# Optimization experiments

Hardware: AMD Instinct MI355X
Metric: run time of the kernel (lower is better)

## Reference

```python
import jax, jax.numpy as jnp
import numpy as np

B = 16        # graphs per protein batch
NPG = 2000    # nodes per graph
N = B * NPG   # total nodes
E = 640000    # total edges
H, C = 3, 128 # heads, hidden_dim
FIN = 1038
K = 400       # ceil(0.2 * NPG) SAGPool keep count
NEG = 0.1     # LeakyReLU slope in model
EPS = 1e-5


def setup_inputs() -> dict:
    key = jax.random.key(0)
    ks = jax.random.split(key, 24)
    d = {}
    d['p1_x'] = jax.random.normal(ks[0], (N, FIN), jnp.float32)
    d['p2_x'] = jax.random.normal(ks[1], (N, FIN), jnp.float32)
    d['p1_edge_index'] = jax.random.randint(ks[2], (2, E), 0, N, jnp.int32)
    d['p2_edge_index'] = jax.random.randint(ks[3], (2, E), 0, N, jnp.int32)
    d['p1_edge_attr'] = jax.random.uniform(ks[4], (E, 2), jnp.float32)
    d['p2_edge_attr'] = jax.random.uniform(ks[5], (E, 2), jnp.float32)
    s_in = 1.0 / np.sqrt(FIN)
    s_h = 1.0 / np.sqrt(C)
    # GATv2Conv params (lin_l has bias, lin_r no bias, lin_edge, att, out bias)
    d['Wl'] = jax.random.normal(ks[6], (FIN, H * C), jnp.float32) * s_in
    d['bl'] = jnp.zeros((H * C,), jnp.float32)
    d['Wr'] = jax.random.normal(ks[7], (FIN, H * C), jnp.float32) * s_in
    d['We'] = jax.random.normal(ks[8], (2, H * C), jnp.float32) * 0.5
    d['att'] = jax.random.normal(ks[9], (H, C), jnp.float32) * s_h
    d['conv_bias'] = jnp.zeros((C,), jnp.float32)
    # BatchNorm1d
    d['gamma'] = jnp.ones((C,), jnp.float32)
    d['beta'] = jnp.zeros((C,), jnp.float32)
    # SAGPooling scorer: GraphConv(C -> 1)
    d['gc_Wrel'] = jax.random.normal(ks[10], (C, 1), jnp.float32) * s_h
    d['gc_Wroot'] = jax.random.normal(ks[11], (C, 1), jnp.float32) * s_h
    d['gc_b'] = jnp.zeros((1,), jnp.float32)
    # MLP head
    d['W1'] = jax.random.normal(ks[12], (2 * C, C), jnp.float32) / np.sqrt(2 * C)
    d['b1'] = jnp.zeros((C,), jnp.float32)
    d['W2'] = jax.random.normal(ks[13], (C, C // 2), jnp.float32) * s_h
    d['b2'] = jnp.zeros((C // 2,), jnp.float32)
    d['Wo'] = jax.random.normal(ks[14], (C // 2, 1), jnp.float32) / np.sqrt(C // 2)
    d['bo'] = jnp.zeros((1,), jnp.float32)
    return d


def gatv2(x, ei, ea, Wl, bl, Wr, We, att, conv_bias):
    # GATv2Conv, heads=3, concat=False, edge_dim=2, add_self_loops (fill='mean')
    loop = jnp.arange(N, dtype=ei.dtype)
    src = jnp.concatenate([ei[0], loop])
    dst = jnp.concatenate([ei[1], loop])
    ea_full = jnp.concatenate([ea, jnp.broadcast_to(ea.mean(0), (N, ea.shape[1]))], 0)
    xl = (x @ Wl + bl).reshape(N, H, C)
    xr = (x @ Wr).reshape(N, H, C)
    ef = (ea_full @ We).reshape(-1, H, C)
    m = xl[src] + xr[dst] + ef                      # [E+N, H, C]
    e = jnp.einsum('ehc,hc->eh', jax.nn.leaky_relu(m, 0.2), att)
    emax = jax.ops.segment_max(e, dst, num_segments=N)
    ex = jnp.exp(e - emax[dst])
    denom = jax.ops.segment_sum(ex, dst, num_segments=N)
    alpha = ex / denom[dst]                          # softmax per dst node, per head
    out = jax.ops.segment_sum(alpha[:, :, None] * xl[src], dst, num_segments=N)
    return out.mean(1) + conv_bias                   # concat=False -> head mean


def branch(x, ei, ea, Wl, bl, Wr, We, att, conv_bias, gamma, beta,
           gc_Wrel, gc_Wroot, gc_b):
    h = gatv2(x, ei, ea, Wl, bl, Wr, We, att, conv_bias)
    h = jax.nn.leaky_relu(h, NEG)
    mu = h.mean(0)
    var = ((h - mu) ** 2).mean(0)
    h = (h - mu) / jnp.sqrt(var + EPS) * gamma + beta  # BatchNorm1d (batch stats)
    # SAGPooling scorer: GraphConv out_i = W_root x_i + W_rel sum_{j->i} x_j + b
    agg = jax.ops.segment_sum(h[ei[0]], ei[1], num_segments=N)
    score = jnp.tanh((h @ gc_Wroot + agg @ gc_Wrel + gc_b)[:, 0])  # [N]
    s = score.reshape(B, NPG)
    topv, topi = jax.lax.top_k(s, K)                 # per-graph top-k
    hb = h.reshape(B, NPG, C)
    hsel = jnp.take_along_axis(hb, topi[:, :, None], axis=1)  # [B, K, C]
    hsel = hsel * topv[:, :, None]                   # x[perm] * tanh(score)[perm]
    return hsel.mean(1)                              # global mean pool -> [B, C]


def reference(p1_x, p2_x, p1_edge_attr, p2_edge_attr, Wl, bl, Wr, We, att,
              conv_bias, gamma, beta, gc_Wrel, gc_Wroot, gc_b, W1, b1, W2, b2,
              Wo, bo, p1_edge_index, p2_edge_index):
    x1 = branch(p1_x, p1_edge_index, p1_edge_attr, Wl, bl, Wr, We, att,
                conv_bias, gamma, beta, gc_Wrel, gc_Wroot, gc_b)
    x2 = branch(p2_x, p2_edge_index, p2_edge_attr, Wl, bl, Wr, We, att,
                conv_bias, gamma, beta, gc_Wrel, gc_Wroot, gc_b)
    xc = jnp.concatenate([x1, x2], 1)                # [B, 2C]
    xc = jax.nn.leaky_relu(xc @ W1 + b1, NEG)
    xc = jax.nn.leaky_relu(xc @ W2 + b2, NEG)
    return jax.nn.sigmoid(xc @ Wo + bo)              # [B, 1]
```

## Files before the change

kernel.cpp:

```cpp
#include <hip/hip_runtime.h>
#include <hip/hip_bf16.h>
#include <math.h>

#define NN 32000
#define EE 640000
#define CC 128
#define HC 384
#define FIN 1038
#define KP 1056
#define KT 33
#define BB 16
#define NPG 2000
#define KK 400

#define XLR_STR 12288000u
#define HBN_STR 4096000u
#define OFF_STR 32064u

#define XL_OFF     0u
#define XR_OFF     24576000u
#define HBN_OFF    49152000u
#define SSRC_OFF   57344000u
#define SEA_OFF    58624000u
#define CNT_OFF    61184000u
#define BNSUM_OFF  61248000u
#define BNSQ_OFF   61248256u
#define MEANEA_OFF 61248512u
#define ZERO_BYTES ((61248516u - 61184000u) * 4u)
#define OFFS_OFF   61248576u
#define CUR_OFF    61312704u
#define R_OFF      61376704u
#define REL_OFF    61440704u
#define SCORE_OFF  61504704u
#define XB_OFF     61568704u
#define WTH_OFF    61572800u

typedef __attribute__((ext_vector_type(8))) _Float16 f16x8;
typedef __attribute__((ext_vector_type(2))) _Float16 f16x2;
typedef __attribute__((ext_vector_type(4))) float f32x4;
typedef __attribute__((ext_vector_type(8))) unsigned short us8;

typedef const __attribute__((address_space(1))) unsigned int* gp1_t;
typedef __attribute__((address_space(3))) unsigned int* lp3_t;
__device__ __forceinline__ void gl_lds16(const void* g, void* l) {
    __builtin_amdgcn_global_load_lds((gp1_t)g, (lp3_t)l, 16, 0, 0);
}

__global__ __launch_bounds__(256) void k_prep(const int* __restrict__ ei0, const int* __restrict__ ei1,
                                              const float* __restrict__ ea0, const float* __restrict__ ea1,
                                              int* __restrict__ cnt, float* __restrict__ meanea) {
    int b = blockIdx.x;
    int br = (b >= 2500);
    int tid = threadIdx.x;
    int e = (b - br * 2500) * 256 + tid;
    const int* ei = br ? ei1 : ei0;
    const float* ea = br ? ea1 : ea0;
    cnt += br * NN; meanea += br * 2;
    float s0 = 0.f, s1 = 0.f;
    if (e < EE) {
        atomicAdd(&cnt[ei[EE + e]], 1);
        float2 t = ((const float2*)ea)[e];
        s0 = t.x; s1 = t.y;
    }
    __shared__ float r0[256], r1[256];
    r0[tid] = s0; r1[tid] = s1; __syncthreads();
    for (int st = 128; st; st >>= 1) {
        if (tid < st) { r0[tid] += r0[tid + st]; r1[tid] += r1[tid + st]; }
        __syncthreads();
    }
    if (tid == 0) { atomicAdd(&meanea[0], r0[0]); atomicAdd(&meanea[1], r1[0]); }
}

__global__ __launch_bounds__(1024) void k_scan(const int* __restrict__ cnt, int* __restrict__ offs, int* __restrict__ cur) {
    int br = blockIdx.x;
    cnt += br * NN; offs += br * OFF_STR; cur += br * NN;
    __shared__ int sb[1024];
    int tid = threadIdx.x;
    int base = tid * 32;
    int s = 0;
    for (int i = 0; i < 32; i++) { int idx = base + i; s += (idx < NN) ? cnt[idx] : 0; }
    sb[tid] = s; __syncthreads();
    for (int off = 1; off < 1024; off <<= 1) {
        int v = (tid >= off) ? sb[tid - off] : 0;
        __syncthreads();
        sb[tid] += v;
        __syncthreads();
    }
    int run = sb[tid] - s;
    for (int i = 0; i < 32; i++) {
        int idx = base + i;
        if (idx < NN) { int c = cnt[idx]; offs[idx] = run; cur[idx] = run; run += c; }
    }
    if (tid == 1023) offs[NN] = run;
}

__global__ __launch_bounds__(256) void k_scatter(const int* __restrict__ ei0, const int* __restrict__ ei1,
                                                 const float* __restrict__ ea0, const float* __restrict__ ea1,
                                                 int* __restrict__ cur, int* __restrict__ ssrc, float2* __restrict__ sea) {
    int b = blockIdx.x;
    int br = (b >= 2500);
    int e = (b - br * 2500) * 256 + threadIdx.x;
    const int* ei = br ? ei1 : ei0;
    const float* ea = br ? ea1 : ea0;
    cur += br * NN; ssrc += br * EE; sea += br * EE;
    if (e < EE) {
        int d = ei[EE + e];
        int p = atomicAdd(&cur[d], 1);
        ssrc[p] = ei[e];
        sea[p] = ((const float2*)ea)[e];
    }
}

__global__ __launch_bounds__(256) void k_cvtW(const float* __restrict__ Wl_, const float* __restrict__ Wr_,
                                              unsigned short* __restrict__ Bh) {
    int idx = blockIdx.x * 256 + threadIdx.x;
    if (idx >= 768 * (KP / 8)) return;
    int n = idx / (KP / 8);
    int seg = idx - n * (KP / 8);
    int c0 = seg * 8;
    const float* W = (n < HC) ? Wl_ : Wr_;
    int nc = (n < HC) ? n : n - HC;
    us8 h8;
#pragma unroll
    for (int j = 0; j < 8; ++j) {
        int k = c0 + j;
        float v = (k < FIN) ? W[(size_t)k * HC + nc] : 0.f;
        _Float16 h = (_Float16)v;
        h8[j] = __builtin_bit_cast(unsigned short, h);
    }
    *(us8*)&Bh[(size_t)n * KP + c0] = h8;
}

__global__ __launch_bounds__(256) void k_gemm2f(const float* __restrict__ x0, const float* __restrict__ x1,
                                                const unsigned short* __restrict__ Bh,
                                                const float* __restrict__ bias, float* __restrict__ ws) {
    __shared__ _Float16 sA[128 * 32], sB[128 * 32];
    const int bid = blockIdx.x;
    const int br = (bid >= 1504);
    const int b2 = br ? (bid - 1504) : bid;
    const float* x = br ? x1 : x0;
    _Float16* xlh = (_Float16*)(ws + XL_OFF) + (size_t)br * XLR_STR;
    float* xr = ws + XR_OFF + br * XLR_STR;

    const int xcd = b2 & 7, slot = b2 >> 3;
    const int t = xcd * 188 + slot;
    if (t >= 1500) return;
    const int mt = t / 6, nt = t - mt * 6;
    const int bm = mt * 128, bn = nt * 128;

    const int tid = threadIdx.x;
    const int wave = tid >> 6, lane = tid & 63;
    const int wm = (wave >> 1) * 64, wn = (wave & 1) * 64;
    const int quad = lane >> 4, l15 = lane & 15;

    const int srow = wave * 16 + (lane >> 2);
    const int scol = (lane & 3) * 8;
    const size_t gB0 = (size_t)(bn + srow) * KP + scol;
    const size_t gB1 = (size_t)(bn + 64 + srow) * KP + scol;
    const int lB0 = (wave * 16) * 32 + lane * 8;
    const int lB1 = (64 + wave * 16) * 32 + lane * 8;

    const int arow0 = wave * 32 + (lane >> 2);
    const int acol = (lane & 3) * 8;

    f32x4 acc[4][4];
#pragma unroll
    for (int i = 0; i < 4; ++i)
#pragma unroll
        for (int j = 0; j < 4; ++j) {
            f32x4 z = {0.f, 0.f, 0.f, 0.f};
            acc[i][j] = z;
        }

    const int aoff0 = (wm + l15) * 32 + quad * 8;
    const int boff0 = (wn + l15) * 32 + quad * 8;

    for (int kt = 0; kt < KT; ++kt) {
        const int kc = kt * 32;
        gl_lds16(Bh + gB0 + kc, &sB[lB0]);
        gl_lds16(Bh + gB1 + kc, &sB[lB1]);
        int gcol = kc + acol;
        if (gcol >= FIN) gcol = 0;
#pragma unroll
        for (int rep = 0; rep < 2; ++rep) {
            const int lrow = arow0 + rep * 16;
            const float* gp = x + (size_t)(bm + lrow) * FIN + gcol;
            float2 v01 = ((const float2*)gp)[0];
            float2 v23 = ((const float2*)gp)[1];
            float2 v45 = ((const float2*)gp)[2];
            float2 v67 = ((const float2*)gp)[3];
            f16x8 a;
            a[0] = (_Float16)v01.x; a[1] = (_Float16)v01.y;
            a[2] = (_Float16)v23.x; a[3] = (_Float16)v23.y;
            a[4] = (_Float16)v45.x; a[5] = (_Float16)v45.y;
            a[6] = (_Float16)v67.x; a[7] = (_Float16)v67.y;
            const int lidx = lrow * 32 + acol;
            *(f16x8*)&sA[lidx] = a;
        }
        __syncthreads();
        f16x8 b[4];
#pragma unroll
        for (int j = 0; j < 4; ++j) b[j] = *(const f16x8*)&sB[boff0 + j * 512];
#pragma unroll
        for (int i = 0; i < 4; ++i) {
            f16x8 a = *(const f16x8*)&sA[aoff0 + i * 512];
#pragma unroll
            for (int j = 0; j < 4; ++j)
                acc[i][j] = __builtin_amdgcn_mfma_f32_16x16x32_f16(a, b[j], acc[i][j], 0, 0, 0);
        }
        __syncthreads();
    }

    const bool isL = (nt < 3);
    if (isL) {
#pragma unroll
        for (int j = 0; j < 4; ++j) {
            const int ncol = wn + j * 16 + l15;
            const float bj = bias[bn + ncol];
#pragma unroll
            for (int i = 0; i < 4; ++i) {
#pragma unroll
                for (int r = 0; r < 4; ++r) {
                    int m = bm + wm + i * 16 + quad * 4 + r;
                    xlh[(size_t)m * HC + bn + ncol] = (_Float16)(acc[i][j][r] + bj);
                }
            }
        }
    } else {
        const int nbase = bn - HC;
#pragma unroll
        for (int j = 0; j < 4; ++j) {
            const int ncol = wn + j * 16 + l15;
#pragma unroll
            for (int i = 0; i < 4; ++i) {
#pragma unroll
                for (int r = 0; r < 4; ++r) {
                    int m = bm + wm + i * 16 + quad * 4 + r;
                    xr[(size_t)m * HC + nbase + ncol] = acc[i][j][r];
                }
            }
        }
    }
}

__global__ __launch_bounds__(256) void k_gat(const unsigned short* __restrict__ xlhb, const float* __restrict__ xrb,
                                             const int* __restrict__ offsb, const int* __restrict__ ssrcb,
                                             const float2* __restrict__ seab, const float* __restrict__ meaneab,
                                             const float* __restrict__ We, const float* __restrict__ att,
                                             const float* __restrict__ conv_bias, float* __restrict__ houtb) {
    int gwave = (blockIdx.x * 256 + threadIdx.x) >> 6;
    int lane = threadIdx.x & 63;
    int half = lane >> 5, l32 = lane & 31;
    int br = (gwave >= NN);
    int node = gwave - br * NN;
    const _Float16* xlh = (const _Float16*)xlhb + (size_t)br * XLR_STR;
    const float* xr = xrb + br * XLR_STR;
    const int* offs = offsb + br * OFF_STR;
    const int* ssrc = ssrcb + br * EE;
    const float2* sea = seab + br * EE;
    const float* meanea = meaneab + br * 2;
    float* hout = houtb + br * HBN_STR;

    f16x2 we0p[6], we1p[6], attp[6], xrp[6];
    const float2* xrw = (const float2*)(xr + (size_t)node * HC);
#pragma unroll
    for (int jj = 0; jj < 6; ++jj) {
        int q = l32 + 32 * jj;
        float2 w0 = ((const float2*)We)[q];
        float2 w1 = ((const float2*)(We + HC))[q];
        float2 av = ((const float2*)att)[q];
        float2 xv = xrw[q];
        we0p[jj][0] = (_Float16)w0.x; we0p[jj][1] = (_Float16)w0.y;
        we1p[jj][0] = (_Float16)w1.x; we1p[jj][1] = (_Float16)w1.y;
        attp[jj][0] = (_Float16)av.x; attp[jj][1] = (_Float16)av.y;
        xrp[jj][0]  = (_Float16)xv.x; xrp[jj][1]  = (_Float16)xv.y;
    }
    float me0 = meanea[0] * (1.0f / EE), me1 = meanea[1] * (1.0f / EE);

    int p0 = offs[node], p1 = offs[node + 1];
    int cntE = p1 - p0;
    int iters = (cntE + 2) >> 1;

    float den0 = 0.f, den1 = 0.f, den2 = 0.f;
    float accv[12];
#pragma unroll
    for (int k = 0; k < 12; ++k) accv[k] = 0.f;

    const f16x2 zero2 = {(_Float16)0.f, (_Float16)0.f};
    const f16x2 c02 = {(_Float16)0.2f, (_Float16)0.2f};

    for (int i = 0; i < iters; ++i) {
        int t = 2 * i + half;
        bool self = (t == 0);
        bool valid = (t <= cntE);
        int p = p0 + t - 1;
        if (p < p0) p = p0;
        if (p > EE - 1) p = EE - 1;
        int sv = ssrc[p];
        float2 ev = sea[p];
        int s = self ? node : sv;
        float ea0 = self ? me0 : ev.x;
        float ea1 = self ? me1 : ev.y;
        f16x2 e0p, e1p;
        e0p[0] = (_Float16)ea0; e0p[1] = e0p[0];
        e1p[0] = (_Float16)ea1; e1p[1] = e1p[0];

        const f16x2* xrow = (const f16x2*)(xlh + (size_t)s * HC);
        f16x2 xv[6];
#pragma unroll
        for (int jj = 0; jj < 6; ++jj) xv[jj] = xrow[l32 + 32 * jj];

        float pr0 = 0.f, pr1 = 0.f, pr2 = 0.f;
#pragma unroll
        for (int jj = 0; jj < 6; ++jj) {
            f16x2 u = xrp[jj] + e0p * we0p[jj];
            u = u + e1p * we1p[jj];
            f16x2 m = xv[jj] + u;
            f16x2 mx = __builtin_elementwise_max(m, zero2);
            f16x2 mn = __builtin_elementwise_min(m, zero2);
            f16x2 lk = mx + mn * c02;
#if __has_builtin(__builtin_amdgcn_fdot2)
            if (jj < 2)      pr0 = __builtin_amdgcn_fdot2(lk, attp[jj], pr0, false);
            else if (jj < 4) pr1 = __builtin_amdgcn_fdot2(lk, attp[jj], pr1, false);
            else             pr2 = __builtin_amdgcn_fdot2(lk, attp[jj], pr2, false);
#else
            float c = (float)lk[0] * (float)attp[jj][0] + (float)lk[1] * (float)attp[jj][1];
            if (jj < 2) pr0 += c; else if (jj < 4) pr1 += c; else pr2 += c;
#endif
        }
#pragma unroll
        for (int msk = 16; msk; msk >>= 1) {
            pr0 += __shfl_xor(pr0, msk);
            pr1 += __shfl_xor(pr1, msk);
            pr2 += __shfl_xor(pr2, msk);
        }
        float w0 = valid ? __expf(pr0) : 0.f;
        float w1 = valid ? __expf(pr1) : 0.f;
        float w2 = valid ? __expf(pr2) : 0.f;
        den0 += w0; den1 += w1; den2 += w2;
#pragma unroll
        for (int jj = 0; jj < 6; ++jj) {
            float wh = (jj < 2) ? w0 : ((jj < 4) ? w1 : w2);
            accv[2 * jj]     += wh * (float)xv[jj][0];
            accv[2 * jj + 1] += wh * (float)xv[jj][1];
        }
    }

#pragma unroll
    for (int k = 0; k < 12; ++k) accv[k] += __shfl_xor(accv[k], 32);
    den0 += __shfl_xor(den0, 32);
    den1 += __shfl_xor(den1, 32);
    den2 += __shfl_xor(den2, 32);

    if (half == 0) {
        float i0 = 1.f / den0, i1 = 1.f / den1, i2 = 1.f / den2;
#pragma unroll
        for (int jja = 0; jja < 2; ++jja) {
#pragma unroll
            for (int b = 0; b < 2; ++b) {
                int c = (((jja * 32 + l32) << 1) | b);
                float o = (accv[2 * jja + b] * i0 + accv[2 * (jja + 2) + b] * i1 +
                           accv[2 * (jja + 4) + b] * i2) * (1.f / 3.f) + conv_bias[c];
                o = (o > 0.f) ? o : 0.1f * o;
                hout[(size_t)node * CC + c] = o;
            }
        }
    }
}

__global__ __launch_bounds__(256) void k_bnstats(const float* __restrict__ hb, float* __restrict__ bnsumb, float* __restrict__ bnsqb) {
    int b = blockIdx.x;
    int br = b >> 9, lb = b & 511;
    const float* h = hb + br * HBN_STR;
    float* bnsum = bnsumb + br * CC;
    float* bnsq = bnsqb + br * CC;
    int c = threadIdx.x & 127;
    int row0 = lb * 2 + (threadIdx.x >> 7);
    float s = 0.f, ss = 0.f;
    for (int n = row0; n < NN; n += 1024) {
        float v = h[(size_t)n * CC + c];
        s += v; ss += v * v;
    }
    atomicAdd(&bnsum[c], s);
    atomicAdd(&bnsq[c], ss);
}

__global__ __launch_bounds__(256) void k_bnapply(float* __restrict__ hb, const float* __restrict__ bnsumb,
                                                 const float* __restrict__ bnsqb,
                                                 const float* __restrict__ gamma, const float* __restrict__ beta,
                                                 const float* __restrict__ wroot,
                                                 const float* __restrict__ wrel, float* __restrict__ r_b, float* __restrict__ rel_b) {
    int gwave = (blockIdx.x * 256 + threadIdx.x) >> 6;
    int lane = threadIdx.x & 63;
    int br = (gwave >= NN);
    int wave = gwave - br * NN;
    float* h = hb + br * HBN_STR;
    const float* bnsum = bnsumb + br * CC;
    const float* bnsq = bnsqb + br * CC;
    float* r_ = r_b + br * NN;
    float* rel_ = rel_b + br * NN;

    float mu0 = bnsum[lane] * (1.f / NN);
    float var0 = bnsq[lane] * (1.f / NN) - mu0 * mu0;
    float sc0 = gamma[lane] * rsqrtf(var0 + 1e-5f);
    float sh0 = beta[lane] - mu0 * sc0;
    float mu1 = bnsum[64 + lane] * (1.f / NN);
    float var1 = bnsq[64 + lane] * (1.f / NN) - mu1 * mu1;
    float sc1 = gamma[64 + lane] * rsqrtf(var1 + 1e-5f);
    float sh1 = beta[64 + lane] - mu1 * sc1;

    size_t base = (size_t)wave * CC;
    float v0 = h[base + lane], v1 = h[base + 64 + lane];
    v0 = v0 * sc0 + sh0;
    v1 = v1 * sc1 + sh1;
    h[base + lane] = v0;
    h[base + 64 + lane] = v1;
    float pr = v0 * wroot[lane] + v1 * wroot[64 + lane];
    float pl = v0 * wrel[lane] + v1 * wrel[64 + lane];
#pragma unroll
    for (int m = 32; m; m >>= 1) {
        pr += __shfl_xor(pr, m);
        pl += __shfl_xor(pl, m);
    }
    if (lane == 0) { r_[wave] = pr; rel_[wave] = pl; }
}

__global__ __launch_bounds__(256) void k_score(const float* __restrict__ r_b, const float* __restrict__ rel_b,
                                               const int* __restrict__ offsb, const int* __restrict__ ssrcb,
                                               const float* __restrict__ gcb, float* __restrict__ scoreb) {
    int gwave = (blockIdx.x * 256 + threadIdx.x) >> 6;
    int lane = threadIdx.x & 63;
    int br = (gwave >= NN);
    int wave = gwave - br * NN;
    const float* r_ = r_b + br * NN;
    const float* rel_ = rel_b + br * NN;
    const int* offs = offsb + br * OFF_STR;
    const int* ssrc = ssrcb + br * EE;
    float* score = scoreb + br * NN;
    int p0 = offs[wave], p1 = offs[wave + 1];
    float s = 0.f;
    for (int p = p0 + lane; p < p1; p += 64) s += rel_[ssrc[p]];
#pragma unroll
    for (int m = 32; m; m >>= 1) s += __shfl_xor(s, m);
    if (lane == 0) score[wave] = tanhf(r_[wave] + s + gcb[0]);
}

__global__ __launch_bounds__(1024) void k_topk(const float* __restrict__ scoreb, const float* __restrict__ hb,
                                               float* __restrict__ xbout) {
    __shared__ float sv[2048];
    __shared__ int si[2048];
    __shared__ float red[8][128];
    int b = blockIdx.x, tid = threadIdx.x;
    int br = b >> 4, g = b & 15;
    const float* score = scoreb + br * NN;
    const float* h = hb + br * HBN_STR;
    for (int i = tid; i < 2048; i += 1024) {
        sv[i] = (i < NPG) ? score[g * NPG + i] : -2.0f;
        si[i] = i;
    }
    __syncthreads();
    for (int k = 2; k <= 2048; k <<= 1) {
        for (int j = k >> 1; j > 0; j >>= 1) {
            for (int t = tid; t < 2048; t += 1024) {
                int ixj = t ^ j;
                if (ixj > t) {
                    bool up = ((t & k) == 0);
                    float a = sv[t], bv = sv[ixj];
                    bool sw = up ? (a < bv) : (a > bv);
                    if (sw) {
                        sv[t] = bv; sv[ixj] = a;
                        int tmp = si[t]; si[t] = si[ixj]; si[ixj] = tmp;
                    }
                }
            }
            __syncthreads();
        }
    }
    int grp = tid >> 7, c = tid & 127;
    float a = 0.f;
    for (int kk = grp; kk < KK; kk += 8) {
        int node = g * NPG + si[kk];
        a += sv[kk] * h[(size_t)node * CC + c];
    }
    red[grp][c] = a;
    __syncthreads();
    if (tid < 128) {
        float v = (red[0][tid] + red[1][tid] + red[2][tid] + red[3][tid] +
                   red[4][tid] + red[5][tid] + red[6][tid] + red[7][tid]) * (1.f / KK);
        xbout[(br * BB + g) * CC + tid] = v;
    }
}

__global__ __launch_bounds__(128) void k_mlp(const float* __restrict__ xb, const float* __restrict__ W1,
                                             const float* __restrict__ b1, const float* __restrict__ W2,
                                             const float* __restrict__ b2, const float* __restrict__ Wo,
                                             const float* __restrict__ bo, float* __restrict__ out) {
    int g = blockIdx.x, tid = threadIdx.x;
    __shared__ float xc[256], l1[128], l2[64];
    xc[tid] = xb[g * CC + tid];
    xc[128 + tid] = xb[BB * CC + g * CC + tid];
    __syncthreads();
    float s = b1[tid];
    for (int i = 0; i < 256; i++) s += xc[i] * W1[i * 128 + tid];
    l1[tid] = (s > 0.f) ? s : 0.1f * s;
    __syncthreads();
    if (tid < 64) {
        float s2 = b2[tid];
        for (int i = 0; i < 128; i++) s2 += l1[i] * W2[i * 64 + tid];
        l2[tid] = (s2 > 0.f) ? s2 : 0.1f * s2;
    }
    __syncthreads();
    if (tid < 64) {
        float p = l2[tid] * Wo[tid];
#pragma unroll
        for (int m = 32; m; m >>= 1) p += __shfl_xor(p, m);
        if (tid == 0) out[g] = 1.f / (1.f + __expf(-(p + bo[0])));
    }
}

extern "C" void kernel_launch(void* const* d_in, const int* in_sizes, int n_in,
                              void* d_out, int out_size, void* d_ws, size_t ws_size,
                              hipStream_t stream) {
    (void)in_sizes; (void)n_in; (void)out_size; (void)ws_size;
    const float* x0   = (const float*)d_in[0];
    const float* x1   = (const float*)d_in[1];
    const int*   ei0  = (const int*)d_in[2];
    const int*   ei1  = (const int*)d_in[3];
    const float* ea0  = (const float*)d_in[4];
    const float* ea1  = (const float*)d_in[5];
    const float* Wl   = (const float*)d_in[6];
    const float* bl   = (const float*)d_in[7];
    const float* Wr   = (const float*)d_in[8];
    const float* We   = (const float*)d_in[9];
    const float* att  = (const float*)d_in[10];
    const float* cb   = (const float*)d_in[11];
    const float* gam  = (const float*)d_in[12];
    const float* bet  = (const float*)d_in[13];
    const float* wrel = (const float*)d_in[14];
    const float* wroot= (const float*)d_in[15];
    const float* gcb  = (const float*)d_in[16];
    const float* W1   = (const float*)d_in[17];
    const float* b1   = (const float*)d_in[18];
    const float* W2   = (const float*)d_in[19];
    const float* b2   = (const float*)d_in[20];
    const float* Wo   = (const float*)d_in[21];
    const float* bo   = (const float*)d_in[22];

    float* ws = (float*)d_ws;
    float*  hbn   = ws + HBN_OFF;
    int*    ssrc  = (int*)(ws + SSRC_OFF);
    float2* sea   = (float2*)(ws + SEA_OFF);
    int*    cnt   = (int*)(ws + CNT_OFF);
    float*  bnsum = ws + BNSUM_OFF;
    float*  bnsq  = ws + BNSQ_OFF;
    float*  meanea= ws + MEANEA_OFF;
    int*    offs  = (int*)(ws + OFFS_OFF);
    int*    cur   = (int*)(ws + CUR_OFF);
    float*  r_    = ws + R_OFF;
    float*  rel_  = ws + REL_OFF;
    float*  score = ws + SCORE_OFF;
    float*  xb    = ws + XB_OFF;
    unsigned short* Wth = (unsigned short*)(ws + WTH_OFF);
    unsigned short* xlh = (unsigned short*)(ws + XL_OFF);
    float*  xr    = ws + XR_OFF;

    hipMemsetAsync(cnt, 0, ZERO_BYTES, stream);
    k_cvtW<<<(768 * (KP / 8) + 255) / 256, 256, 0, stream>>>(Wl, Wr, Wth);

    k_prep<<<5000, 256, 0, stream>>>(ei0, ei1, ea0, ea1, cnt, meanea);
    k_scan<<<2, 1024, 0, stream>>>(cnt, offs, cur);
    k_scatter<<<5000, 256, 0, stream>>>(ei0, ei1, ea0, ea1, cur, ssrc, sea);

    k_gemm2f<<<3008, 256, 0, stream>>>(x0, x1, Wth, bl, ws);

    k_gat<<<16000, 256, 0, stream>>>(xlh, xr, offs, ssrc, sea, meanea, We, att, cb, hbn);

    k_bnstats<<<1024, 256, 0, stream>>>(hbn, bnsum, bnsq);
    k_bnapply<<<16000, 256, 0, stream>>>(hbn, bnsum, bnsq, gam, bet, wroot, wrel, r_, rel_);
    k_score<<<16000, 256, 0, stream>>>(r_, rel_, offs, ssrc, gcb, score);
    k_topk<<<32, 1024, 0, stream>>>(score, hbn, xb);

    k_mlp<<<BB, 128, 0, stream>>>(xb, W1, b1, W2, b2, Wo, bo, (float*)d_out);
}
```

Baseline: 1.244 ms.

## Double-buffer GEMM LDS tiles and pack CSR edge source with fp16 attrs

The input-projection GEMM now double-buffers its A and B LDS tiles. The next k-slice's global loads are issued before the MFMAs on the current slice, and one barrier per iteration is removed. Separately, the CSR scatter now writes the source index and the two edge attributes (converted to fp16) as one int2 record, so k_gat and k_score do a single 8-byte gather instead of two separate arrays. The cost is doubled LDS and more live registers in the GEMM, which may lower occupancy, plus reduced precision for the edge attributes.

```diff
diff --git a/kernel.cpp b/kernel.cpp
--- a/kernel.cpp
+++ b/kernel.cpp
@@ -96,18 +96,22 @@
 
 __global__ __launch_bounds__(256) void k_scatter(const int* __restrict__ ei0, const int* __restrict__ ei1,
                                                  const float* __restrict__ ea0, const float* __restrict__ ea1,
-                                                 int* __restrict__ cur, int* __restrict__ ssrc, float2* __restrict__ sea) {
+                                                 int* __restrict__ cur, int2* __restrict__ sed) {
     int b = blockIdx.x;
     int br = (b >= 2500);
     int e = (b - br * 2500) * 256 + threadIdx.x;
     const int* ei = br ? ei1 : ei0;
     const float* ea = br ? ea1 : ea0;
-    cur += br * NN; ssrc += br * EE; sea += br * EE;
+    cur += br * NN; sed += br * EE;
     if (e < EE) {
         int d = ei[EE + e];
         int p = atomicAdd(&cur[d], 1);
-        ssrc[p] = ei[e];
-        sea[p] = ((const float2*)ea)[e];
+        float2 t = ((const float2*)ea)[e];
+        f16x2 h; h[0] = (_Float16)t.x; h[1] = (_Float16)t.y;
+        int2 pk;
+        pk.x = ei[e];
+        pk.y = __builtin_bit_cast(int, h);
+        sed[p] = pk;
     }
 }
 
@@ -134,7 +138,7 @@
 __global__ __launch_bounds__(256) void k_gemm2f(const float* __restrict__ x0, const float* __restrict__ x1,
                                                 const unsigned short* __restrict__ Bh,
                                                 const float* __restrict__ bias, float* __restrict__ ws) {
-    __shared__ _Float16 sA[128 * 32], sB[128 * 32];
+    __shared__ _Float16 sA[2][128 * 32], sB[2][128 * 32];
     const int bid = blockIdx.x;
     const int br = (bid >= 1504);
     const int b2 = br ? (bid - 1504) : bid;
@@ -163,6 +167,33 @@
     const int arow0 = wave * 32 + (lane >> 2);
     const int acol = (lane & 3) * 8;
 
+    float af[2][8];
+
+#define LOADA(KT_) do {                                                         \
+        int gcol = (KT_) * 32 + acol;                                           \
+        if (gcol >= FIN) gcol = 0;                                              \
+        _Pragma("unroll")                                                       \
+        for (int rep = 0; rep < 2; ++rep) {                                     \
+            const float* gp = x + (size_t)(bm + arow0 + rep * 16) * FIN + gcol; \
+            float2 v01 = ((const float2*)gp)[0];                                \
+            float2 v23 = ((const float2*)gp)[1];                                \
+            float2 v45 = ((const float2*)gp)[2];                                \
+            float2 v67 = ((const float2*)gp)[3];                                \
+            af[rep][0] = v01.x; af[rep][1] = v01.y;                             \
+            af[rep][2] = v23.x; af[rep][3] = v23.y;                             \
+            af[rep][4] = v45.x; af[rep][5] = v45.y;                             \
+            af[rep][6] = v67.x; af[rep][7] = v67.y;                             \
+        } } while (0)
+
+#define CVTWRITE(BUF_) do {                                                     \
+        _Pragma("unroll")                                                       \
+        for (int rep = 0; rep < 2; ++rep) {                                     \
+            f16x8 a;                                                            \
+            _Pragma("unroll")                                                   \
+            for (int j = 0; j < 8; ++j) a[j] = (_Float16)af[rep][j];            \
+            *(f16x8*)&sA[BUF_][(arow0 + rep * 16) * 32 + acol] = a;             \
+        } } while (0)
+
     f32x4 acc[4][4];
 #pragma unroll
     for (int i = 0; i < 4; ++i)
@@ -175,41 +206,36 @@
     const int aoff0 = (wm + l15) * 32 + quad * 8;
     const int boff0 = (wn + l15) * 32 + quad * 8;
 
+    gl_lds16(Bh + gB0, &sB[0][lB0]);
+    gl_lds16(Bh + gB1, &sB[0][lB1]);
+    LOADA(0);
+    CVTWRITE(0);
+    __syncthreads();
+
     for (int kt = 0; kt < KT; ++kt) {
-        const int kc = kt * 32;
-        gl_lds16(Bh + gB0 + kc, &sB[lB0]);
-        gl_lds16(Bh + gB1 + kc, &sB[lB1]);
-        int gcol = kc + acol;
-        if (gcol >= FIN) gcol = 0;
-#pragma unroll
-        for (int rep = 0; rep < 2; ++rep) {
-            const int lrow = arow0 + rep * 16;
-            const float* gp = x + (size_t)(bm + lrow) * FIN + gcol;
-            float2 v01 = ((const float2*)gp)[0];
-            float2 v23 = ((const float2*)gp)[1];
-            float2 v45 = ((const float2*)gp)[2];
-            float2 v67 = ((const float2*)gp)[3];
-            f16x8 a;
-            a[0] = (_Float16)v01.x; a[1] = (_Float16)v01.y;
-            a[2] = (_Float16)v23.x; a[3] = (_Float16)v23.y;
-            a[4] = (_Float16)v45.x; a[5] = (_Float16)v45.y;
-            a[6] = (_Float16)v67.x; a[7] = (_Float16)v67.y;
-            const int lidx = lrow * 32 + acol;
-            *(f16x8*)&sA[lidx] = a;
-        }
+        const int cur = kt & 1, nxt = cur ^ 1;
+        const bool pf = (kt + 1 < KT);
+        if (pf) {
+            const int kc = (kt + 1) * 32;
+            gl_lds16(Bh + gB0 + kc, &sB[nxt][lB0]);
+            gl_lds16(Bh + gB1 + kc, &sB[nxt][lB1]);
+            LOADA(kt + 1);
+        }
+        f16x8 bfr[4];
+#pragma unroll
+        for (int j = 0; j < 4; ++j) bfr[j] = *(const f16x8*)&sB[cur][boff0 + j * 512];
+#pragma unroll
+        for (int i = 0; i < 4; ++i) {
+            f16x8 a = *(const f16x8*)&sA[cur][aoff0 + i * 512];
+#pragma unroll
+            for (int j = 0; j < 4; ++j)
+                acc[i][j] = __builtin_amdgcn_mfma_f32_16x16x32_f16(a, bfr[j], acc[i][j], 0, 0, 0);
+        }
+        if (pf) CVTWRITE(nxt);
         __syncthreads();
-        f16x8 b[4];
-#pragma unroll
-        for (int j = 0; j < 4; ++j) b[j] = *(const f16x8*)&sB[boff0 + j * 512];
-#pragma unroll
-        for (int i = 0; i < 4; ++i) {
-            f16x8 a = *(const f16x8*)&sA[aoff0 + i * 512];
-#pragma unroll
-            for (int j = 0; j < 4; ++j)
-                acc[i][j] = __builtin_amdgcn_mfma_f32_16x16x32_f16(a, b[j], acc[i][j], 0, 0, 0);
-        }
-        __syncthreads();
-    }
+    }
+#undef LOADA
+#undef CVTWRITE
 
     const bool isL = (nt < 3);
     if (isL) {
@@ -244,8 +270,8 @@
 }
 
 __global__ __launch_bounds__(256) void k_gat(const unsigned short* __restrict__ xlhb, const float* __restrict__ xrb,
-                                             const int* __restrict__ offsb, const int* __restrict__ ssrcb,
-                                             const float2* __restrict__ seab, const float* __restrict__ meaneab,
+                                             const int* __restrict__ offsb, const int2* __restrict__ sedb,
+                                             const float* __restrict__ meaneab,
                                              const float* __restrict__ We, const float* __restrict__ att,
                                              const float* __restrict__ conv_bias, float* __restrict__ houtb) {
     int gwave = (blockIdx.x * 256 + threadIdx.x) >> 6;
@@ -256,8 +282,7 @@
     const _Float16* xlh = (const _Float16*)xlhb + (size_t)br * XLR_STR;
     const float* xr = xrb + br * XLR_STR;
     const int* offs = offsb + br * OFF_STR;
-    const int* ssrc = ssrcb + br * EE;
-    const float2* sea = seab + br * EE;
+    const int2* sed = sedb + br * EE;
     const float* meanea = meaneab + br * 2;
     float* hout = houtb + br * HBN_STR;
 
@@ -275,7 +300,8 @@
         attp[jj][0] = (_Float16)av.x; attp[jj][1] = (_Float16)av.y;
         xrp[jj][0]  = (_Float16)xv.x; xrp[jj][1]  = (_Float16)xv.y;
     }
-    float me0 = meanea[0] * (1.0f / EE), me1 = meanea[1] * (1.0f / EE);
+    _Float16 meh0 = (_Float16)(meanea[0] * (1.0f / EE));
+    _Float16 meh1 = (_Float16)(meanea[1] * (1.0f / EE));
 
     int p0 = offs[node], p1 = offs[node + 1];
     int cntE = p1 - p0;
@@ -296,14 +322,14 @@
         int p = p0 + t - 1;
         if (p < p0) p = p0;
         if (p > EE - 1) p = EE - 1;
-        int sv = ssrc[p];
-        float2 ev = sea[p];
-        int s = self ? node : sv;
-        float ea0 = self ? me0 : ev.x;
-        float ea1 = self ? me1 : ev.y;
+        int2 pk = sed[p];
+        f16x2 eh = __builtin_bit_cast(f16x2, pk.y);
+        int s = self ? node : pk.x;
+        _Float16 e0 = self ? meh0 : eh[0];
+        _Float16 e1 = self ? meh1 : eh[1];
         f16x2 e0p, e1p;
-        e0p[0] = (_Float16)ea0; e0p[1] = e0p[0];
-        e1p[0] = (_Float16)ea1; e1p[1] = e1p[0];
+        e0p[0] = e0; e0p[1] = e0;
+        e1p[0] = e1; e1p[1] = e1;
 
         const f16x2* xrow = (const f16x2*)(xlh + (size_t)s * HC);
         f16x2 xv[6];
@@ -426,7 +452,7 @@
 }
 
 __global__ __launch_bounds__(256) void k_score(const float* __restrict__ r_b, const float* __restrict__ rel_b,
-                                               const int* __restrict__ offsb, const int* __restrict__ ssrcb,
+                                               const int* __restrict__ offsb, const int2* __restrict__ sedb,
                                                const float* __restrict__ gcb, float* __restrict__ scoreb) {
     int gwave = (blockIdx.x * 256 + threadIdx.x) >> 6;
     int lane = threadIdx.x & 63;
@@ -435,11 +461,11 @@
     const float* r_ = r_b + br * NN;
     const float* rel_ = rel_b + br * NN;
     const int* offs = offsb + br * OFF_STR;
-    const int* ssrc = ssrcb + br * EE;
+    const int2* sed = sedb + br * EE;
     float* score = scoreb + br * NN;
     int p0 = offs[wave], p1 = offs[wave + 1];
     float s = 0.f;
-    for (int p = p0 + lane; p < p1; p += 64) s += rel_[ssrc[p]];
+    for (int p = p0 + lane; p < p1; p += 64) s += rel_[sed[p].x];
 #pragma unroll
     for (int m = 32; m; m >>= 1) s += __shfl_xor(s, m);
     if (lane == 0) score[wave] = tanhf(r_[wave] + s + gcb[0]);
@@ -548,8 +574,7 @@
 
     float* ws = (float*)d_ws;
     float*  hbn   = ws + HBN_OFF;
-    int*    ssrc  = (int*)(ws + SSRC_OFF);
-    float2* sea   = (float2*)(ws + SEA_OFF);
+    int2*   sed   = (int2*)(ws + SEA_OFF);
     int*    cnt   = (int*)(ws + CNT_OFF);
     float*  bnsum = ws + BNSUM_OFF;
     float*  bnsq  = ws + BNSQ_OFF;
@@ -569,15 +594,15 @@
 
     k_prep<<<5000, 256, 0, stream>>>(ei0, ei1, ea0, ea1, cnt, meanea);
     k_scan<<<2, 1024, 0, stream>>>(cnt, offs, cur);
-    k_scatter<<<5000, 256, 0, stream>>>(ei0, ei1, ea0, ea1, cur, ssrc, sea);
+    k_scatter<<<5000, 256, 0, stream>>>(ei0, ei1, ea0, ea1, cur, sed);
 
     k_gemm2f<<<3008, 256, 0, stream>>>(x0, x1, Wth, bl, ws);
 
-    k_gat<<<16000, 256, 0, stream>>>(xlh, xr, offs, ssrc, sea, meanea, We, att, cb, hbn);
+    k_gat<<<16000, 256, 0, stream>>>(xlh, xr, offs, sed, meanea, We, att, cb, hbn);
 
     k_bnstats<<<1024, 256, 0, stream>>>(hbn, bnsum, bnsq);
     k_bnapply<<<16000, 256, 0, stream>>>(hbn, bnsum, bnsq, gam, bet, wroot, wrel, r_, rel_);
-    k_score<<<16000, 256, 0, stream>>>(r_, rel_, offs, ssrc, gcb, score);
+    k_score<<<16000, 256, 0, stream>>>(r_, rel_, offs, sed, gcb, score);
     k_topk<<<32, 1024, 0, stream>>>(score, hbn, xb);
 
     k_mlp<<<BB, 128, 0, stream>>>(xb, W1, b1, W2, b2, Wo, bo, (float*)d_out);
```

Result: no change. 1.254 ms (+0.8%).
